# Kernel optimization log

Measured on AMD Instinct MI355X. Metric: run time of the kernel, lower is better.

The kernel has to match this reference:

```python
import jax, jax.numpy as jnp
import numpy as np

EPS = 1e-5

def _ln(t, g, b):
    m = t.mean(-1, keepdims=True)
    v = ((t - m) ** 2).mean(-1, keepdims=True)
    return (t - m) * jax.lax.rsqrt(v + EPS) * g + b

def _sr(t, w, b, H, W, sr):
    # t: [B, H*W, C] -> spatial-reduction conv -> [B, (H//sr)*(W//sr), C]
    B, L, C = t.shape
    xi = t.transpose(0, 2, 1).reshape(B, C, H, W)
    y = jax.lax.conv_general_dilated(xi, w, (sr, sr), 'VALID',
                                     dimension_numbers=('NCHW', 'OIHW', 'NCHW'))
    return y.reshape(B, C, -1).transpose(0, 2, 1) + b

def setup_inputs() -> dict:
    key = jax.random.key(0)
    ks = jax.random.split(key, 9)
    C, head, sr, H, W = 128, 2, 2, 64, 64
    B, N = 4, 2 * H * W
    s = 0.02
    return {
        'x': jax.random.normal(ks[0], (B, N, C), jnp.float32),
        'qW': jax.random.normal(ks[1], (C, C), jnp.float32) * s,
        'qb': jnp.zeros((C,), jnp.float32),
        'kvW': jax.random.normal(ks[2], (C, 2 * C), jnp.float32) * s,
        'kvb': jnp.zeros((2 * C,), jnp.float32),
        'projW': jax.random.normal(ks[3], (C, C), jnp.float32) * s,
        'projb': jnp.zeros((C,), jnp.float32),
        'srW': jax.random.normal(ks[4], (C, C, sr, sr), jnp.float32) * s,
        'srb': jnp.zeros((C,), jnp.float32),
        'lnW': jnp.ones((C,), jnp.float32),
        'lnB': jnp.zeros((C,), jnp.float32),
        'H': H, 'W': W, 'fuse': 1,
    }

def reference(x, qW, qb, kvW, kvb, projW, projb, srW, srb, lnW, lnB, H, W, fuse):
    head, sr = 2, 2
    B, N, C = x.shape
    Dh = C // head
    scale = Dh ** -0.5
    q = (x @ qW + qb).reshape(B, N, head, Dh).transpose(0, 2, 1, 3)  # [B,h,N,Dh]
    mask = None
    if fuse and sr > 1:
        half = N // 2
        x_rgb = _ln(_sr(x[:, :half, :], srW, srb, H, W, sr), lnW, lnB)
        x_dte = _ln(_sr(x[:, half:, :], srW, srb, H, W, sr), lnW, lnB)
        xkv = jnp.concatenate([x_rgb, x_dte], axis=1)
        M = N // (sr * sr)
        row = jnp.arange(N)[:, None] < half            # query in rgb half
        col = jnp.arange(M)[None, :] < (M // 2)        # key in rgb half
        mask = row == col                              # True on same-modality blocks -> masked
    elif sr > 1:
        xkv = _ln(_sr(x, srW, srb, H, W, sr), lnW, lnB)
    else:
        xkv = x
    M = xkv.shape[1]
    kv = (xkv @ kvW + kvb).reshape(B, M, 2, head, Dh).transpose(2, 0, 3, 1, 4)
    k, v = kv[0], kv[1]                                # [B,h,M,Dh]
    attn = jnp.einsum('bhnd,bhmd->bhnm', q, k) * scale
    if mask is not None:
        attn = jnp.where(mask[None, None], -jnp.inf, attn)
    attn = jax.nn.softmax(attn, axis=-1)
    out = jnp.einsum('bhnm,bhmd->bhnd', attn, v).transpose(0, 2, 1, 3).reshape(B, N, C)
    return out @ projW + projb
```

## Files before the change

kernel.cpp:

```cpp
#include <hip/hip_runtime.h>
#include <hip/hip_bf16.h>

#define LN_EPS 1e-5f

typedef __attribute__((ext_vector_type(8))) short bf16x8_t;
typedef __attribute__((ext_vector_type(4))) float f32x4_t;
typedef __attribute__((ext_vector_type(4))) unsigned short u16x4_t;

#define MFMA32(a, b, c) __builtin_amdgcn_mfma_f32_16x16x32_bf16(a, b, c, 0, 0, 0)

__device__ inline float fast_exp2(float x) {
#if __has_builtin(__builtin_amdgcn_exp2f)
    return __builtin_amdgcn_exp2f(x);
#else
    float r;
    asm volatile("v_exp_f32 %0, %1\n\ts_nop 0" : "=v"(r) : "v"(x));
    return r;
#endif
}

__device__ inline unsigned short f2bf(float f) {
    union { float f; unsigned int u; } v; v.f = f;
    unsigned int r = v.u + 0x7fffu + ((v.u >> 16) & 1u);
    return (unsigned short)(r >> 16);
}

__device__ inline u16x4_t pk4(float a, float b, float c, float d) {
    union { u16x4_t v; __hip_bfloat162 h[2]; } u;
    u.h[0] = __float22bfloat162_rn(float2{a, b});
    u.h[1] = __float22bfloat162_rn(float2{c, d});
    return u.v;
}
__device__ inline bf16x8_t pk8(float4 a, float4 b) {
    union { bf16x8_t v; __hip_bfloat162 h[4]; } u;
    u.h[0] = __float22bfloat162_rn(float2{a.x, a.y});
    u.h[1] = __float22bfloat162_rn(float2{a.z, a.w});
    u.h[2] = __float22bfloat162_rn(float2{b.x, b.y});
    u.h[3] = __float22bfloat162_rn(float2{b.z, b.w});
    return u.v;
}

__device__ inline size_t fragidx(int row, int k, int KC) {
    return ((size_t)((row >> 4) * KC + (k >> 5))) * 512 +
           (((k >> 3) & 3) * 16 + (row & 15)) * 8 + (k & 7);
}

__global__ void k_prep_w(const float* __restrict__ qW, const float* __restrict__ kvW,
                         const float* __restrict__ projW, const float* __restrict__ srW,
                         unsigned short* __restrict__ qWs, unsigned short* __restrict__ kvWs,
                         unsigned short* __restrict__ projWs, unsigned short* __restrict__ srWs) {
    int i = blockIdx.x * 256 + threadIdx.x;
    if (i < 16384) {
        int n = i & 127, k = i >> 7;
        qWs[fragidx(n, k, 4)] = f2bf(qW[k * 128 + n]);
    } else if (i < 49152) {
        int j = i - 16384; int n = j & 255, k = j >> 8;
        kvWs[fragidx(n, k, 4)] = f2bf(kvW[k * 256 + n]);
    } else if (i < 65536) {
        int j = i - 49152; int n = j & 127, k = j >> 7;
        projWs[fragidx(n, k, 4)] = f2bf(projW[k * 128 + n]);
    } else {
        int j = i - 65536; int n = j >> 9, rem = j & 511, q = rem >> 7, c = rem & 127;
        srWs[fragidx(n, q * 128 + c, 16)] = f2bf(srW[n * 512 + c * 4 + q]);
    }
}

#define XPAD 132
__global__ __launch_bounds__(256)
void k_convkv(const float* __restrict__ x, const unsigned short* __restrict__ srWs,
              const float* __restrict__ srb, const float* __restrict__ lnW,
              const float* __restrict__ lnB, const unsigned short* __restrict__ kvWs,
              const float* __restrict__ kvb, unsigned short* __restrict__ ksw,
              unsigned short* __restrict__ vls) {
    const int t = threadIdx.x, w = t >> 6, lane = t & 63;
    const int col = lane & 15, quad = lane >> 4;
    const int RT = blockIdx.x;

    __shared__ unsigned short xl[64 * XPAD];
    __shared__ unsigned short xs[4 * 512];
    __shared__ float lnred[4][16][2];

    const int pb = RT >> 7, phf = (RT >> 6) & 1;
    const int oy = (RT >> 1) & 31, ox0 = (RT & 1) * 16;
    const int n0 = phf * 4096 + 2 * oy * 64 + 2 * ox0;
    #pragma unroll
    for (int it = 0; it < 8; it++) {
        int idx = it * 256 + t;
        int chunk = idx >> 10;
        int rr = (idx >> 5) & 31;
        int c4 = idx & 31;
        float4 v = *(const float4*)(x + ((size_t)(pb * 8192 + n0 + chunk * 64 + rr)) * 128 + c4 * 4);
        *(u16x4_t*)(xl + (chunk * 32 + rr) * XPAD + c4 * 4) = pk4(v.x, v.y, v.z, v.w);
    }
    __syncthreads();

    f32x4_t acc[2] = {};
    {
        const unsigned short* wp = srWs + lane * 8;
        #pragma unroll
        for (int kc = 0; kc < 16; kc++) {
            const int q = kc >> 2, cg = kc & 3;
            const int r = (q >> 1) * 32 + 2 * col + (q & 1);
            bf16x8_t xb = *(const bf16x8_t*)(xl + r * XPAD + cg * 32 + quad * 8);
            #pragma unroll
            for (int jj = 0; jj < 2; jj++) {
                bf16x8_t wf = *(const bf16x8_t*)(wp + (size_t)((w * 2 + jj) * 16 + kc) * 512);
                acc[jj] = MFMA32(wf, xb, acc[jj]);
            }
        }
    }
    float s = 0.f, ss = 0.f;
    #pragma unroll
    for (int jj = 0; jj < 2; jj++) {
        float4 bs = *(const float4*)(srb + (w * 2 + jj) * 16 + quad * 4);
        acc[jj][0] += bs.x; acc[jj][1] += bs.y; acc[jj][2] += bs.z; acc[jj][3] += bs.w;
        #pragma unroll
        for (int r = 0; r < 4; r++) { float v = acc[jj][r]; s += v; ss += v * v; }
    }
    s += __shfl_xor(s, 16, 64);  s += __shfl_xor(s, 32, 64);
    ss += __shfl_xor(ss, 16, 64); ss += __shfl_xor(ss, 32, 64);
    if (lane < 16) { lnred[w][lane][0] = s; lnred[w][lane][1] = ss; }
    __syncthreads();
    float stot = 0.f, sstot = 0.f;
    #pragma unroll
    for (int ww = 0; ww < 4; ww++) { stot += lnred[ww][col][0]; sstot += lnred[ww][col][1]; }
    float mean = stot * (1.0f / 128.0f);
    float var = sstot * (1.0f / 128.0f) - mean * mean;
    float rs = rsqrtf(var + LN_EPS);
    #pragma unroll
    for (int jj = 0; jj < 2; jj++) {
        int f0 = (w * 2 + jj) * 16 + quad * 4;
        float4 g = *(const float4*)(lnW + f0);
        float4 be = *(const float4*)(lnB + f0);
        u16x4_t o = pk4((acc[jj][0] - mean) * rs * g.x + be.x,
                        (acc[jj][1] - mean) * rs * g.y + be.y,
                        (acc[jj][2] - mean) * rs * g.z + be.z,
                        (acc[jj][3] - mean) * rs * g.w + be.w);
        *(u16x4_t*)(xs + ((size_t)(f0 >> 5)) * 512 +
                    (((f0 >> 3) & 3) * 16 + col) * 8 + (f0 & 7)) = o;
    }
    __syncthreads();
    bf16x8_t xf[4];
    #pragma unroll
    for (int kc = 0; kc < 4; kc++)
        xf[kc] = *(const bf16x8_t*)(xs + (size_t)kc * 512 + lane * 8);
    const int p0 = RT * 16;
    const int bb = p0 >> 11;
    #pragma unroll
    for (int jj = 0; jj < 2; jj++) {
        const int nt = w * 2 + jj;
        f32x4_t aK = {};
        #pragma unroll
        for (int kc = 0; kc < 4; kc++) {
            bf16x8_t wf = *(const bf16x8_t*)(kvWs + (size_t)(nt * 4 + kc) * 512 + lane * 8);
            aK = MFMA32(wf, xf[kc], aK);
        }
        float4 bs = *(const float4*)(kvb + nt * 16 + quad * 4);
        int m = (p0 + col) & 2047;
        int bh = bb * 2 + (nt >> 2);
        int d0 = (nt & 3) * 16 + quad * 4;
        u16x4_t o = pk4(aK[0] + bs.x, aK[1] + bs.y, aK[2] + bs.z, aK[3] + bs.w);
        *(u16x4_t*)(ksw + ((size_t)(bh * 128 + (m >> 4)) * 2 + (d0 >> 5)) * 512 +
                    (((d0 >> 3) & 3) * 16 + (m & 15)) * 8 + (d0 & 7)) = o;
    }
    #pragma unroll
    for (int jj = 0; jj < 2; jj++) {
        const int nt = w * 2 + jj;
        f32x4_t aV = {};
        #pragma unroll
        for (int kc = 0; kc < 4; kc++) {
            bf16x8_t wf = *(const bf16x8_t*)(kvWs + (size_t)((8 + nt) * 4 + kc) * 512 + lane * 8);
            aV = MFMA32(xf[kc], wf, aV);
        }
        int fv = nt * 16 + col;
        int h = fv >> 6, dd = fv & 63;
        float bv = kvb[128 + fv];
        int m0 = (p0 + quad * 4) & 2047;
        int bh = bb * 2 + h;
        int kt = m0 >> 6;
        int tt = (m0 >> 5) & 1;
        int base = m0 & 31;
        int quad_b = base >> 3, j0 = base & 7;
        u16x4_t o = pk4(aV[0] + bv, aV[1] + bv, aV[2] + bv, aV[3] + bv);
        *(u16x4_t*)(vls + (((size_t)((bh * 32 + kt) * 4 + (dd >> 4)) * 2 + tt) * 512) +
                    (quad_b * 16 + (dd & 15)) * 8 + j0) = o;
    }
}

__global__ __launch_bounds__(256, 2)
void k_attn_f10(const float* __restrict__ x, const unsigned short* __restrict__ qWs,
                const float* __restrict__ qb, const unsigned short* __restrict__ ksw,
                const unsigned short* __restrict__ vls, const unsigned short* __restrict__ projWs,
                const float* __restrict__ projb, float* __restrict__ out) {
    const int blkx = blockIdx.x, mod = blockIdx.y, b = blockIdx.z;
    const int t = threadIdx.x, w = t >> 6, lane = t & 63;
    const int col = lane & 15, quad = lane >> 4;
    const int ks = w & 1, h = w >> 1;
    const int bh = b * 2 + h;
    const int qbase = mod * 4096 + blkx * 64;

    __shared__ char arena[35200];
    unsigned short* qstage = (unsigned short*)arena;
    unsigned short* pw     = (unsigned short*)arena + w * 2048;
    unsigned short* rows   = (unsigned short*)arena;
    float* Ocomb = (float*)(arena + 17536);
    float* lcomb = (float*)(arena + 34944);

    const float sc = 0.125f * 1.44269504089f;
    #pragma unroll
    for (int qtl = 0; qtl < 2; qtl++) {
        const int qt = ks * 2 + qtl;
        const float* xrow = x + ((size_t)b * 8192 + qbase + qt * 16 + col) * 128;
        f32x4_t acc[4] = {};
        #pragma unroll
        for (int kc = 0; kc < 4; kc++) {
            float4 xa = *(const float4*)(xrow + kc * 32 + quad * 8);
            float4 xb2 = *(const float4*)(xrow + kc * 32 + quad * 8 + 4);
            bf16x8_t xf = pk8(xa, xb2);
            #pragma unroll
            for (int j = 0; j < 4; j++) {
                bf16x8_t wf = *(const bf16x8_t*)(qWs + (size_t)((h * 4 + j) * 4 + kc) * 512 + lane * 8);
                acc[j] = MFMA32(wf, xf, acc[j]);
            }
        }
        #pragma unroll
        for (int j = 0; j < 4; j++) {
            float4 bs = *(const float4*)(qb + h * 64 + j * 16 + quad * 4);
            u16x4_t o = pk4((acc[j][0] + bs.x) * sc, (acc[j][1] + bs.y) * sc,
                            (acc[j][2] + bs.z) * sc, (acc[j][3] + bs.w) * sc);
            *(u16x4_t*)(qstage + (size_t)h * 4096 + ((size_t)(qt * 2 + (j >> 1))) * 512 +
                        (((j & 1) * 2 + (quad >> 1)) * 16 + col) * 8 + (quad & 1) * 4) = o;
        }
    }
    __syncthreads();
    bf16x8_t qf[4][2];
    #pragma unroll
    for (int qt = 0; qt < 4; qt++)
        #pragma unroll
        for (int kc = 0; kc < 2; kc++)
            qf[qt][kc] = *(const bf16x8_t*)(qstage + (size_t)h * 4096 +
                                            (size_t)(qt * 2 + kc) * 512 + lane * 8);
    __syncthreads();

    const unsigned short* kp0 =
        ksw + ((size_t)(bh * 128 + (1 - mod) * 64) * 2) * 512 + lane * 8;
    const unsigned short* vp0 =
        vls + ((size_t)((bh * 32 + (1 - mod) * 16) * 8)) * 512 + lane * 8;
    const bf16x8_t ones8 = { 0x3F80, 0x3F80, 0x3F80, 0x3F80,
                             0x3F80, 0x3F80, 0x3F80, 0x3F80 };

    f32x4_t O[4][4] = {};
    f32x4_t accl[4] = {};

    for (int kti = 0; kti < 8; kti++) {
        const int kt = ks * 8 + kti;
        bf16x8_t kf[8], vf[8];
        #pragma unroll
        for (int i = 0; i < 8; i++) {
            kf[i] = *(const bf16x8_t*)(kp0 + (size_t)(kt * 8 + i) * 512);
            vf[i] = *(const bf16x8_t*)(vp0 + (size_t)(kt * 8 + i) * 512);
        }
        #pragma unroll
        for (int qp = 0; qp < 2; qp++) {
            f32x4_t ST[2][4];
            #pragma unroll
            for (int qtl = 0; qtl < 2; qtl++) {
                const int qt = qp * 2 + qtl;
                #pragma unroll
                for (int nb = 0; nb < 4; nb++) {
                    f32x4_t sA = {};
                    sA = MFMA32(kf[nb * 2 + 0], qf[qt][0], sA);
                    sA = MFMA32(kf[nb * 2 + 1], qf[qt][1], sA);
                    ST[qtl][nb] = sA;
                }
            }
            #pragma unroll
            for (int qtl = 0; qtl < 2; qtl++)
                #pragma unroll
                for (int nb = 0; nb < 4; nb++) {
                    u16x4_t pk = pk4(fast_exp2(ST[qtl][nb][0]), fast_exp2(ST[qtl][nb][1]),
                                     fast_exp2(ST[qtl][nb][2]), fast_exp2(ST[qtl][nb][3]));
                    *(u16x4_t*)(pw + qtl * 1024 + (nb >> 1) * 512 +
                                (((nb & 1) * 2 + (quad >> 1)) * 16 + col) * 8 + (quad & 1) * 4) = pk;
                }
            #pragma unroll
            for (int qtl = 0; qtl < 2; qtl++) {
                const int qt = qp * 2 + qtl;
                bf16x8_t pf0 = *(const bf16x8_t*)(pw + qtl * 1024 + lane * 8);
                bf16x8_t pf1 = *(const bf16x8_t*)(pw + qtl * 1024 + 512 + lane * 8);
                accl[qt] = MFMA32(pf0, ones8, accl[qt]);
                accl[qt] = MFMA32(pf1, ones8, accl[qt]);
                #pragma unroll
                for (int dt = 0; dt < 4; dt++) {
                    O[qt][dt] = MFMA32(pf0, vf[dt * 2 + 0], O[qt][dt]);
                    O[qt][dt] = MFMA32(pf1, vf[dt * 2 + 1], O[qt][dt]);
                }
            }
        }
    }
    __syncthreads();

    #pragma unroll
    for (int hp = 0; hp < 2; hp++) {
        if (h == hp && ks == 1) {
            #pragma unroll
            for (int qt = 0; qt < 4; qt++)
                #pragma unroll
                for (int r = 0; r < 4; r++) {
                    int qrow = qt * 16 + quad * 4 + r;
                    #pragma unroll
                    for (int dt = 0; dt < 4; dt++)
                        Ocomb[qrow * 68 + dt * 16 + col] = O[qt][dt][r];
                    if (col == 0) lcomb[qrow] = accl[qt][r];
                }
        }
        __syncthreads();
        if (h == hp && ks == 0) {
            #pragma unroll
            for (int qt = 0; qt < 4; qt++)
                #pragma unroll
                for (int r = 0; r < 4; r++) {
                    int qrow = qt * 16 + quad * 4 + r;
                    float lt = accl[qt][r] + lcomb[qrow];
                    float rl = 1.0f / lt;
                    #pragma unroll
                    for (int dt = 0; dt < 4; dt++) {
                        float ov = O[qt][dt][r] + Ocomb[qrow * 68 + dt * 16 + col];
                        rows[qrow * 136 + hp * 64 + dt * 16 + col] = f2bf(ov * rl);
                    }
                }
        }
        __syncthreads();
    }

    {
        const int qt2 = w;
        bf16x8_t ob[4];
        #pragma unroll
        for (int kc = 0; kc < 4; kc++)
            ob[kc] = *(const bf16x8_t*)(rows + (size_t)(qt2 * 16 + col) * 136 + kc * 32 + quad * 8);
        f32x4_t acc[8];
        #pragma unroll
        for (int j = 0; j < 8; j++) acc[j] = f32x4_t{};
        #pragma unroll
        for (int kc = 0; kc < 4; kc++)
            #pragma unroll
            for (int j = 0; j < 8; j++) {
                bf16x8_t wf = *(const bf16x8_t*)(projWs + (size_t)(j * 4 + kc) * 512 + lane * 8);
                acc[j] = MFMA32(wf, ob[kc], acc[j]);
            }
        const int n = b * 8192 + qbase + qt2 * 16 + col;
        #pragma unroll
        for (int j = 0; j < 8; j++) {
            int f0 = j * 16 + quad * 4;
            float4 bs = *(const float4*)(projb + f0);
            float4 o = { acc[j][0] + bs.x, acc[j][1] + bs.y,
                         acc[j][2] + bs.z, acc[j][3] + bs.w };
            *(float4*)(out + (size_t)n * 128 + f0) = o;
        }
    }
}

extern "C" void kernel_launch(void* const* d_in, const int* in_sizes, int n_in,
                              void* d_out, int out_size, void* d_ws, size_t ws_size,
                              hipStream_t stream) {
    const float* x     = (const float*)d_in[0];
    const float* qW    = (const float*)d_in[1];
    const float* qb    = (const float*)d_in[2];
    const float* kvW   = (const float*)d_in[3];
    const float* kvb   = (const float*)d_in[4];
    const float* projW = (const float*)d_in[5];
    const float* projb = (const float*)d_in[6];
    const float* srW   = (const float*)d_in[7];
    const float* srb   = (const float*)d_in[8];
    const float* lnW   = (const float*)d_in[9];
    const float* lnB   = (const float*)d_in[10];

    char* ws = (char*)d_ws;
    unsigned short* qWs    = (unsigned short*)(ws + 0);
    unsigned short* kvWs   = (unsigned short*)(ws + 32768);
    unsigned short* projWs = (unsigned short*)(ws + 98304);
    unsigned short* srWs   = (unsigned short*)(ws + 131072);
    unsigned short* ksw    = (unsigned short*)(ws + 262144);
    unsigned short* vls    = (unsigned short*)(ws + 2359296);

    k_prep_w<<<dim3(512), dim3(256), 0, stream>>>(qW, kvW, projW, srW,
                                                  qWs, kvWs, projWs, srWs);
    k_convkv<<<dim3(512), dim3(256), 0, stream>>>(x, srWs, srb, lnW, lnB,
                                                  kvWs, kvb, ksw, vls);
    k_attn_f10<<<dim3(64, 2, 4), dim3(256), 0, stream>>>(x, qWs, qb, ksw, vls,
                                                         projWs, projb, (float*)d_out);
}
```

Baseline: 132.8 us.

## Double-buffer K/V register loads and interleave score and PV MFMA phases

The attention inner loop now holds two register buffers of K/V fragments, so the loads for the next key tile are issued before the current tile is computed. Each tile body is also reordered: the score MFMAs for the second query pair are issued before the PV MFMAs of the first pair, which spreads exp2 and LDS work between matrix operations. The aim is to hide global-load latency and keep the MFMA pipe busier. The cost is roughly 64 more VGPRs per lane, which could cause spills or limit occupancy under the 2-blocks-per-CU launch bound.

```diff
diff --git a/kernel.cpp b/kernel.cpp
--- a/kernel.cpp
+++ b/kernel.cpp
@@ -188,7 +188,7 @@
 }
 
 __global__ __launch_bounds__(256, 2)
-void k_attn_f10(const float* __restrict__ x, const unsigned short* __restrict__ qWs,
+void k_attn_f11(const float* __restrict__ x, const unsigned short* __restrict__ qWs,
                 const float* __restrict__ qb, const unsigned short* __restrict__ ksw,
                 const unsigned short* __restrict__ vls, const unsigned short* __restrict__ projWs,
                 const float* __restrict__ projb, float* __restrict__ out) {
@@ -252,51 +252,96 @@
     f32x4_t O[4][4] = {};
     f32x4_t accl[4] = {};
 
-    for (int kti = 0; kti < 8; kti++) {
-        const int kt = ks * 8 + kti;
-        bf16x8_t kf[8], vf[8];
+    bf16x8_t kfA[8], vfA[8], kfB[8], vfB[8];
+    const int ktbase = ks * 8;
+
+    auto prefA = [&](int kt) {
         #pragma unroll
         for (int i = 0; i < 8; i++) {
-            kf[i] = *(const bf16x8_t*)(kp0 + (size_t)(kt * 8 + i) * 512);
-            vf[i] = *(const bf16x8_t*)(vp0 + (size_t)(kt * 8 + i) * 512);
-        }
-        #pragma unroll
-        for (int qp = 0; qp < 2; qp++) {
-            f32x4_t ST[2][4];
-            #pragma unroll
-            for (int qtl = 0; qtl < 2; qtl++) {
-                const int qt = qp * 2 + qtl;
-                #pragma unroll
-                for (int nb = 0; nb < 4; nb++) {
-                    f32x4_t sA = {};
-                    sA = MFMA32(kf[nb * 2 + 0], qf[qt][0], sA);
-                    sA = MFMA32(kf[nb * 2 + 1], qf[qt][1], sA);
-                    ST[qtl][nb] = sA;
-                }
-            }
-            #pragma unroll
-            for (int qtl = 0; qtl < 2; qtl++)
-                #pragma unroll
-                for (int nb = 0; nb < 4; nb++) {
-                    u16x4_t pk = pk4(fast_exp2(ST[qtl][nb][0]), fast_exp2(ST[qtl][nb][1]),
-                                     fast_exp2(ST[qtl][nb][2]), fast_exp2(ST[qtl][nb][3]));
-                    *(u16x4_t*)(pw + qtl * 1024 + (nb >> 1) * 512 +
-                                (((nb & 1) * 2 + (quad >> 1)) * 16 + col) * 8 + (quad & 1) * 4) = pk;
-                }
-            #pragma unroll
-            for (int qtl = 0; qtl < 2; qtl++) {
-                const int qt = qp * 2 + qtl;
-                bf16x8_t pf0 = *(const bf16x8_t*)(pw + qtl * 1024 + lane * 8);
-                bf16x8_t pf1 = *(const bf16x8_t*)(pw + qtl * 1024 + 512 + lane * 8);
-                accl[qt] = MFMA32(pf0, ones8, accl[qt]);
-                accl[qt] = MFMA32(pf1, ones8, accl[qt]);
-                #pragma unroll
-                for (int dt = 0; dt < 4; dt++) {
-                    O[qt][dt] = MFMA32(pf0, vf[dt * 2 + 0], O[qt][dt]);
-                    O[qt][dt] = MFMA32(pf1, vf[dt * 2 + 1], O[qt][dt]);
-                }
-            }
-        }
+            kfA[i] = *(const bf16x8_t*)(kp0 + (size_t)(kt * 8 + i) * 512);
+            vfA[i] = *(const bf16x8_t*)(vp0 + (size_t)(kt * 8 + i) * 512);
+        }
+    };
+    auto prefB = [&](int kt) {
+        #pragma unroll
+        for (int i = 0; i < 8; i++) {
+            kfB[i] = *(const bf16x8_t*)(kp0 + (size_t)(kt * 8 + i) * 512);
+            vfB[i] = *(const bf16x8_t*)(vp0 + (size_t)(kt * 8 + i) * 512);
+        }
+    };
+    auto body = [&](bf16x8_t (&kfc)[8], bf16x8_t (&vfc)[8]) {
+        f32x4_t ST0[2][4];
+        #pragma unroll
+        for (int qtl = 0; qtl < 2; qtl++)
+            #pragma unroll
+            for (int nb = 0; nb < 4; nb++) {
+                f32x4_t sA = {};
+                sA = MFMA32(kfc[nb * 2 + 0], qf[qtl][0], sA);
+                sA = MFMA32(kfc[nb * 2 + 1], qf[qtl][1], sA);
+                ST0[qtl][nb] = sA;
+            }
+        #pragma unroll
+        for (int qtl = 0; qtl < 2; qtl++)
+            #pragma unroll
+            for (int nb = 0; nb < 4; nb++) {
+                u16x4_t pk = pk4(fast_exp2(ST0[qtl][nb][0]), fast_exp2(ST0[qtl][nb][1]),
+                                 fast_exp2(ST0[qtl][nb][2]), fast_exp2(ST0[qtl][nb][3]));
+                *(u16x4_t*)(pw + qtl * 1024 + (nb >> 1) * 512 +
+                            (((nb & 1) * 2 + (quad >> 1)) * 16 + col) * 8 + (quad & 1) * 4) = pk;
+            }
+        f32x4_t ST1[2][4];
+        #pragma unroll
+        for (int qtl = 0; qtl < 2; qtl++)
+            #pragma unroll
+            for (int nb = 0; nb < 4; nb++) {
+                f32x4_t sA = {};
+                sA = MFMA32(kfc[nb * 2 + 0], qf[2 + qtl][0], sA);
+                sA = MFMA32(kfc[nb * 2 + 1], qf[2 + qtl][1], sA);
+                ST1[qtl][nb] = sA;
+            }
+        #pragma unroll
+        for (int qtl = 0; qtl < 2; qtl++) {
+            bf16x8_t pf0 = *(const bf16x8_t*)(pw + qtl * 1024 + lane * 8);
+            bf16x8_t pf1 = *(const bf16x8_t*)(pw + qtl * 1024 + 512 + lane * 8);
+            accl[qtl] = MFMA32(pf0, ones8, accl[qtl]);
+            accl[qtl] = MFMA32(pf1, ones8, accl[qtl]);
+            #pragma unroll
+            for (int dt = 0; dt < 4; dt++) {
+                O[qtl][dt] = MFMA32(pf0, vfc[dt * 2 + 0], O[qtl][dt]);
+                O[qtl][dt] = MFMA32(pf1, vfc[dt * 2 + 1], O[qtl][dt]);
+            }
+        }
+        #pragma unroll
+        for (int qtl = 0; qtl < 2; qtl++)
+            #pragma unroll
+            for (int nb = 0; nb < 4; nb++) {
+                u16x4_t pk = pk4(fast_exp2(ST1[qtl][nb][0]), fast_exp2(ST1[qtl][nb][1]),
+                                 fast_exp2(ST1[qtl][nb][2]), fast_exp2(ST1[qtl][nb][3]));
+                *(u16x4_t*)(pw + qtl * 1024 + (nb >> 1) * 512 +
+                            (((nb & 1) * 2 + (quad >> 1)) * 16 + col) * 8 + (quad & 1) * 4) = pk;
+            }
+        #pragma unroll
+        for (int qtl = 0; qtl < 2; qtl++) {
+            const int qt = 2 + qtl;
+            bf16x8_t pf0 = *(const bf16x8_t*)(pw + qtl * 1024 + lane * 8);
+            bf16x8_t pf1 = *(const bf16x8_t*)(pw + qtl * 1024 + 512 + lane * 8);
+            accl[qt] = MFMA32(pf0, ones8, accl[qt]);
+            accl[qt] = MFMA32(pf1, ones8, accl[qt]);
+            #pragma unroll
+            for (int dt = 0; dt < 4; dt++) {
+                O[qt][dt] = MFMA32(pf0, vfc[dt * 2 + 0], O[qt][dt]);
+                O[qt][dt] = MFMA32(pf1, vfc[dt * 2 + 1], O[qt][dt]);
+            }
+        }
+    };
+
+    prefA(ktbase);
+    #pragma unroll
+    for (int kt2 = 0; kt2 < 4; kt2++) {
+        prefB(ktbase + kt2 * 2 + 1);
+        body(kfA, vfA);
+        if (kt2 < 3) prefA(ktbase + kt2 * 2 + 2);
+        body(kfB, vfB);
     }
     __syncthreads();
 
@@ -388,6 +433,6 @@
                                                   qWs, kvWs, projWs, srWs);
     k_convkv<<<dim3(512), dim3(256), 0, stream>>>(x, srWs, srb, lnW, lnB,
                                                   kvWs, kvb, ksw, vls);
-    k_attn_f10<<<dim3(64, 2, 4), dim3(256), 0, stream>>>(x, qWs, qb, ksw, vls,
+    k_attn_f11<<<dim3(64, 2, 4), dim3(256), 0, stream>>>(x, qWs, qb, ksw, vls,
                                                          projWs, projb, (float*)d_out);
 }
```

Result: faster. 129.3 us (-2.6%).
